# Optimization experiments

Hardware: AMD Instinct MI355X
Metric: run time of the kernel (lower is better)

The kernel has to match this reference:

```python
import jax, jax.numpy as jnp
import numpy as np

N_POINTS = 12288
FEAT_DIM = 16


def setup_inputs() -> dict:
    key = jax.random.key(0)
    feats = jax.random.normal(key, (N_POINTS, FEAT_DIM), dtype=jnp.float32)
    return {"feats": feats, "topK": 1}


def reference(feats, topK):
    """LOGG3D_ATTN eval path for a single point cloud (batch=1).

    feats: [N, D] post-spvcnn point features.
    1) self_attention -> scalar weight per point
    2) weight features, top-k select k = N*topK points
    3) SOP: mean second-order (outer-product) pooling, flatten, L2-normalize.
    """
    N, D = feats.shape
    inv_sqrt_d = 1.0 / jnp.sqrt(jnp.asarray(D, feats.dtype))
    # self-attention over points: [N, N] scores (the ridge-regime hot spot)
    scores = jnp.matmul(feats, feats.T) * inv_sqrt_d          # [N, N]
    attn = jax.nn.softmax(scores, axis=-1)                    # [N, N]
    ctx = jnp.matmul(attn, feats)                             # [N, D]
    weights = jax.nn.sigmoid(jnp.sum(ctx * feats, axis=-1, keepdims=True))  # [N, 1]

    weighted_feat = feats * weights                           # [N, D]
    k = int(N * topK)
    _, top_idx = jax.lax.top_k(weights[:, 0], k)              # [k]
    x = weighted_feat[top_idx][None, :, :]                    # [1, k, D]

    # SOP: mean outer-product pooling (signed_sqrt=False, do_fc=False)
    so = jnp.einsum('bnd,bne->bde', x, x) / k                 # [1, D, D]
    out = so.reshape(1, -1)                                   # [1, D*D]
    out = out / jnp.linalg.norm(out, axis=-1, keepdims=True)
    return out
```

## Files before the change

kernel.cpp:

```cpp
#include <hip/hip_runtime.h>
#include <hip/hip_bf16.h>
#include <math.h>


#define NP 12288
#define JSPLIT 16
#define JCHUNK (NP / JSPLIT)
#define JT 384
#define NTILES (JCHUNK / JT)
#define JGPT (JT / 16)

#define QSCALE 0.3606737602222839f

typedef __attribute__((ext_vector_type(4))) float f32x4;
typedef __attribute__((ext_vector_type(2))) unsigned u32x2;
typedef __attribute__((ext_vector_type(8))) short s16x8;
typedef __attribute__((ext_vector_type(4))) short s16x4;

#if defined(__has_builtin)
#if __has_builtin(__builtin_amdgcn_mfma_f32_16x16x16bf16_1k)
#define HAVE_MFMA16_BUILTIN 1
#endif
#if __has_builtin(__builtin_amdgcn_exp2f)
#define EXP2F(x) __builtin_amdgcn_exp2f(x)
#endif
#endif
#ifndef EXP2F
#define EXP2F(x) exp2f(x)
#endif

static __device__ __forceinline__ f32x4 mfma16(s16x4 a, s16x4 b, f32x4 c) {
#ifdef HAVE_MFMA16_BUILTIN
    return __builtin_amdgcn_mfma_f32_16x16x16bf16_1k(a, b, c, 0, 0, 0);
#else
    f32x4 d;
    asm volatile("s_nop 1\n\t"
                 "v_mfma_f32_16x16x16_bf16 %0, %1, %2, %0"
                 : "=v"(d)
                 : "v"(a), "v"(b), "0"(c));
    return d;
#endif
}

static __device__ __forceinline__ short f2bf(float x) {
    __hip_bfloat16 h = __float2bfloat16(x);
    return __builtin_bit_cast(short, h);
}

static __device__ __forceinline__ s16x4 pack_rhu(f32x4 e) {
    const unsigned u0 = __builtin_bit_cast(unsigned, e[0]) + 0x8000u;
    const unsigned u1 = __builtin_bit_cast(unsigned, e[1]) + 0x8000u;
    const unsigned u2 = __builtin_bit_cast(unsigned, e[2]) + 0x8000u;
    const unsigned u3 = __builtin_bit_cast(unsigned, e[3]) + 0x8000u;
    u32x2 t;
    t[0] = (u0 >> 16) | (u1 & 0xFFFF0000u);
    t[1] = (u2 >> 16) | (u3 & 0xFFFF0000u);
    return __builtin_bit_cast(s16x4, t);
}

__global__ __launch_bounds__(256)
void prep(const float* __restrict__ feats,
          unsigned short* __restrict__ ghi, unsigned short* __restrict__ shi,
          unsigned short* __restrict__ gFt)
{
    __shared__ unsigned short tr[64 * 16];
    const int tid = threadIdx.x;
    const int rowbase = blockIdx.x * 64;

    const f32x4 v = *(const f32x4*)(feats + (size_t)rowbase * 16 + tid * 4);
    s16x4 hv, sv;
    #pragma unroll
    for (int k = 0; k < 4; ++k) {
        hv[k] = f2bf(v[k]);
        sv[k] = f2bf(v[k] * QSCALE);
    }
    *(s16x4*)(ghi + (size_t)rowbase * 16 + tid * 4) = hv;
    *(s16x4*)(shi + (size_t)rowbase * 16 + tid * 4) = sv;
    *(s16x4*)(tr + (tid >> 2) * 16 + (tid & 3) * 4) = hv;
    __syncthreads();

    if (tid < 128) {
        const int p = tid >> 3, q8 = tid & 7;
        s16x8 o;
        #pragma unroll
        for (int e = 0; e < 8; ++e) o[e] = (short)tr[(q8 * 8 + e) * 16 + p];
        *(s16x8*)(gFt + (size_t)p * NP + rowbase + q8 * 8) = o;
    }
}

__global__ __launch_bounds__(256)
void attn_mfma(const unsigned short* __restrict__ ghi,
               const unsigned short* __restrict__ shi,
               const unsigned short* __restrict__ gFt,
               float* __restrict__ ctx_part,
               float* __restrict__ l_part)
{
    __shared__ unsigned short hiT[JT * 16];
    __shared__ unsigned short FtT[16 * JT];

    const int tid = threadIdx.x;
    const int wave = tid >> 6, lane = tid & 63;
    const int il = lane & 15, g = lane >> 4, g4 = g * 4, g8 = g * 8;
    const int js = blockIdx.x & (JSPLIT - 1);
    const int rowblk = blockIdx.x >> 4;
    const int ibase = rowblk * 128 + wave * 32;
    const int jbase = js * JCHUNK;

    const s16x4 bA = *(const s16x4*)(shi + (size_t)(ibase + il) * 16 + g4);
    const s16x4 bB = *(const s16x4*)(shi + (size_t)(ibase + 16 + il) * 16 + g4);

    s16x4 ones; ones[0] = ones[1] = ones[2] = ones[3] = (short)0x3F80;
    const f32x4 kZero = {0.f, 0.f, 0.f, 0.f};
    f32x4 ctxA = kZero, ctxB = kZero, lA = kZero, lB = kZero;

    const char* aBase = (const char*)hiT + ((il * 32 + g8) ^ ((il & 7) << 4));
    const char* vPlane = (const char*)FtT + il * (JT * 2);
    const int vKey = (il & 7) << 4;

    const int fp = tid >> 4, fq = tid & 15;

    for (int ti = 0; ti < NTILES; ++ti) {
        const int jb = jbase + ti * JT;
        {
            const char* gH = (const char*)ghi + (size_t)jb * 32;
            #pragma unroll
            for (int k = 0; k < 3; ++k) {
                const int c = tid + (k << 8);
                s16x8 v = *(const s16x8*)(gH + c * 16);
                *(s16x8*)((char*)hiT + ((c * 16) ^ (((c >> 1) & 7) << 4))) = v;
            }
            const char* gF = (const char*)gFt + (size_t)fp * (NP * 2) + (size_t)jb * 2;
            #pragma unroll
            for (int k = 0; k < 3; ++k) {
                const int cq = fq + (k << 4);
                s16x8 v = *(const s16x8*)(gF + cq * 16);
                *(s16x8*)((char*)FtT + fp * (JT * 2)
                          + ((cq * 16) ^ ((fp & 7) << 4))) = v;
            }
        }
        __syncthreads();

        #pragma unroll 4
        for (int jg = 0; jg < JGPT; ++jg) {
            const s16x4 aS = *(const s16x4*)(aBase + jg * 512);
            const s16x4 aV = *(const s16x4*)(vPlane + (((jg << 5) + g8) ^ vKey));
            const f32x4 sa = mfma16(aS, bA, kZero);
            const f32x4 sb = mfma16(aS, bB, kZero);
            f32x4 ea, eb;
            ea[0] = EXP2F(sa[0]); ea[1] = EXP2F(sa[1]);
            ea[2] = EXP2F(sa[2]); ea[3] = EXP2F(sa[3]);
            eb[0] = EXP2F(sb[0]); eb[1] = EXP2F(sb[1]);
            eb[2] = EXP2F(sb[2]); eb[3] = EXP2F(sb[3]);
            const s16x4 pA = pack_rhu(ea);
            const s16x4 pB = pack_rhu(eb);
            ctxA = mfma16(aV, pA, ctxA);
            lA   = mfma16(ones, pA, lA);
            ctxB = mfma16(aV, pB, ctxB);
            lB   = mfma16(ones, pB, lB);
        }
        __syncthreads();
    }

    asm volatile("s_nop 7\n\ts_nop 7" ::: );

    const int iA = ibase + il, iB = iA + 16;
    *(f32x4*)(ctx_part + ((size_t)js * NP + iA) * 16 + g4) = ctxA;
    *(f32x4*)(ctx_part + ((size_t)js * NP + iB) * 16 + g4) = ctxB;
    if (g == 0) {
        l_part[(size_t)js * NP + iA] = lA[0];
        l_part[(size_t)js * NP + iB] = lB[0];
    }
}

__global__ __launch_bounds__(256)
void weights_sop(const float* __restrict__ feats,
                 const float* __restrict__ ctxp,
                 const float* __restrict__ lp,
                 float* __restrict__ mpart)
{
    __shared__ float gw[64 * 16];
    const int tid = threadIdx.x;
    const int rl = tid >> 2, q = tid & 3, d0 = q * 4;
    const int row = blockIdx.x * 64 + rl;

    f32x4 c = {0.f, 0.f, 0.f, 0.f};
    float l = 0.f;
    #pragma unroll
    for (int js = 0; js < JSPLIT; ++js) {
        c += *(const f32x4*)(ctxp + ((size_t)js * NP + row) * 16 + d0);
        l += lp[(size_t)js * NP + row];
    }
    const f32x4 fv = *(const f32x4*)(feats + (size_t)row * 16 + d0);
    float zp = c[0]*fv[0] + c[1]*fv[1] + c[2]*fv[2] + c[3]*fv[3];
    zp += __shfl_xor(zp, 1, 64);
    zp += __shfl_xor(zp, 2, 64);
    const float z = zp / l;
    const float w = 1.f / (1.f + EXP2F(-z * 1.4426950408889634f));

    f32x4 gv; gv[0] = w*fv[0]; gv[1] = w*fv[1]; gv[2] = w*fv[2]; gv[3] = w*fv[3];
    *(f32x4*)(gw + rl * 16 + d0) = gv;
    __syncthreads();

    const int d = tid >> 4, e = tid & 15;
    float acc = 0.f;
    #pragma unroll 8
    for (int r = 0; r < 64; ++r)
        acc += gw[r * 16 + d] * gw[r * 16 + e];
    mpart[(size_t)blockIdx.x * 256 + tid] = acc;
}

__global__ __launch_bounds__(1024)
void finalize(const float* __restrict__ mpart, float* __restrict__ out)
{
    __shared__ float part[1024];
    __shared__ float red[4];
    const int tid = threadIdx.x;
    const int o = tid & 255, s = tid >> 8;

    float m = 0.f;
    #pragma unroll 4
    for (int b = s; b < 192; b += 4) m += mpart[(size_t)b * 256 + o];
    part[tid] = m;
    __syncthreads();

    if (tid < 256) {
        m = part[tid] + part[tid + 256] + part[tid + 512] + part[tid + 768];
        float ss = m * m;
        #pragma unroll
        for (int msk = 32; msk >= 1; msk >>= 1) ss += __shfl_xor(ss, msk, 64);
        if ((tid & 63) == 0) red[tid >> 6] = ss;
    }
    __syncthreads();
    if (tid < 256) {
        const float tot = red[0] + red[1] + red[2] + red[3];
        out[tid] = m / sqrtf(tot);
    }
}

extern "C" void kernel_launch(void* const* d_in, const int* in_sizes, int n_in,
                              void* d_out, int out_size, void* d_ws, size_t ws_size,
                              hipStream_t stream) {
    (void)n_in; (void)out_size; (void)ws_size;
    const float* feats = (const float*)d_in[0];

    char* w = (char*)d_ws;
    unsigned short* ghi = (unsigned short*)(w);
    unsigned short* shi = (unsigned short*)(w + 393216);
    unsigned short* gFt = (unsigned short*)(w + 786432);
    float* ctxp = (float*)(w + 1179648);
    float* lp   = (float*)(w + 13762560);
    float* mp   = (float*)(w + 14548992);

    prep       <<<192,  256, 0, stream>>>(feats, ghi, shi, gFt);
    attn_mfma  <<<1536, 256, 0, stream>>>(ghi, shi, gFt, ctxp, lp);
    weights_sop<<<192,  256, 0, stream>>>(feats, ctxp, lp, mp);
    finalize   <<<1,    1024, 0, stream>>>(mp, (float*)d_out);
}
```

Measured before the change: 87.77 us.

## Drop LDS staging in attention kernel and load operands directly from global

Removes the shared-memory tiles and the per-tile __syncthreads, so each wave reads its bf16 score and value operands straight from global memory (L1/L2) inside a single loop over the whole j-chunk. This cuts LDS write/read traffic and barrier stalls. The cost is redundant global loads, since the four waves in a block each fetch the same j data, and the loads are 8-byte and strided. The bf16 packing also switches to a v_perm byte permute in place of shift/mask/or.

```diff
diff --git a/kernel.cpp b/kernel.cpp
--- a/kernel.cpp
+++ b/kernel.cpp
@@ -6,9 +6,7 @@
 #define NP 12288
 #define JSPLIT 16
 #define JCHUNK (NP / JSPLIT)
-#define JT 384
-#define NTILES (JCHUNK / JT)
-#define JGPT (JT / 16)
+#define JGTOT (JCHUNK / 16)
 
 #define QSCALE 0.3606737602222839f
 
@@ -23,6 +21,9 @@
 #endif
 #if __has_builtin(__builtin_amdgcn_exp2f)
 #define EXP2F(x) __builtin_amdgcn_exp2f(x)
+#endif
+#if __has_builtin(__builtin_amdgcn_perm)
+#define HAVE_PERM 1
 #endif
 #endif
 #ifndef EXP2F
@@ -53,9 +54,21 @@
     const unsigned u2 = __builtin_bit_cast(unsigned, e[2]) + 0x8000u;
     const unsigned u3 = __builtin_bit_cast(unsigned, e[3]) + 0x8000u;
     u32x2 t;
+#ifdef HAVE_PERM
+    t[0] = __builtin_amdgcn_perm(u1, u0, 0x07060302u);
+    t[1] = __builtin_amdgcn_perm(u3, u2, 0x07060302u);
+#else
     t[0] = (u0 >> 16) | (u1 & 0xFFFF0000u);
     t[1] = (u2 >> 16) | (u3 & 0xFFFF0000u);
+#endif
     return __builtin_bit_cast(s16x4, t);
+}
+
+static __device__ __forceinline__ f32x4 exp4(f32x4 s) {
+    f32x4 e;
+    e[0] = EXP2F(s[0]); e[1] = EXP2F(s[1]);
+    e[2] = EXP2F(s[2]); e[3] = EXP2F(s[3]);
+    return e;
 }
 
 __global__ __launch_bounds__(256)
@@ -95,9 +108,6 @@
                float* __restrict__ ctx_part,
                float* __restrict__ l_part)
 {
-    __shared__ unsigned short hiT[JT * 16];
-    __shared__ unsigned short FtT[16 * JT];
-
     const int tid = threadIdx.x;
     const int wave = tid >> 6, lane = tid & 63;
     const int il = lane & 15, g = lane >> 4, g4 = g * 4, g8 = g * 8;
@@ -113,52 +123,22 @@
     const f32x4 kZero = {0.f, 0.f, 0.f, 0.f};
     f32x4 ctxA = kZero, ctxB = kZero, lA = kZero, lB = kZero;
 
-    const char* aBase = (const char*)hiT + ((il * 32 + g8) ^ ((il & 7) << 4));
-    const char* vPlane = (const char*)FtT + il * (JT * 2);
-    const int vKey = (il & 7) << 4;
-
-    const int fp = tid >> 4, fq = tid & 15;
-
-    for (int ti = 0; ti < NTILES; ++ti) {
-        const int jb = jbase + ti * JT;
-        {
-            const char* gH = (const char*)ghi + (size_t)jb * 32;
-            #pragma unroll
-            for (int k = 0; k < 3; ++k) {
-                const int c = tid + (k << 8);
-                s16x8 v = *(const s16x8*)(gH + c * 16);
-                *(s16x8*)((char*)hiT + ((c * 16) ^ (((c >> 1) & 7) << 4))) = v;
-            }
-            const char* gF = (const char*)gFt + (size_t)fp * (NP * 2) + (size_t)jb * 2;
-            #pragma unroll
-            for (int k = 0; k < 3; ++k) {
-                const int cq = fq + (k << 4);
-                s16x8 v = *(const s16x8*)(gF + cq * 16);
-                *(s16x8*)((char*)FtT + fp * (JT * 2)
-                          + ((cq * 16) ^ ((fp & 7) << 4))) = v;
-            }
-        }
-        __syncthreads();
-
-        #pragma unroll 4
-        for (int jg = 0; jg < JGPT; ++jg) {
-            const s16x4 aS = *(const s16x4*)(aBase + jg * 512);
-            const s16x4 aV = *(const s16x4*)(vPlane + (((jg << 5) + g8) ^ vKey));
-            const f32x4 sa = mfma16(aS, bA, kZero);
-            const f32x4 sb = mfma16(aS, bB, kZero);
-            f32x4 ea, eb;
-            ea[0] = EXP2F(sa[0]); ea[1] = EXP2F(sa[1]);
-            ea[2] = EXP2F(sa[2]); ea[3] = EXP2F(sa[3]);
-            eb[0] = EXP2F(sb[0]); eb[1] = EXP2F(sb[1]);
-            eb[2] = EXP2F(sb[2]); eb[3] = EXP2F(sb[3]);
-            const s16x4 pA = pack_rhu(ea);
-            const s16x4 pB = pack_rhu(eb);
-            ctxA = mfma16(aV, pA, ctxA);
-            lA   = mfma16(ones, pA, lA);
-            ctxB = mfma16(aV, pB, ctxB);
-            lB   = mfma16(ones, pB, lB);
-        }
-        __syncthreads();
+    const char* pS = (const char*)ghi + (size_t)(jbase + il) * 32 + g8;
+    const char* pV = (const char*)gFt + (size_t)il * (NP * 2)
+                     + (size_t)jbase * 2 + g8;
+
+    #pragma unroll 4
+    for (int jg = 0; jg < JGTOT; ++jg) {
+        const s16x4 aS = *(const s16x4*)(pS + (size_t)jg * 512);
+        const s16x4 aV = *(const s16x4*)(pV + (size_t)jg * 32);
+        const f32x4 sa = mfma16(aS, bA, kZero);
+        const f32x4 sb = mfma16(aS, bB, kZero);
+        const s16x4 pA = pack_rhu(exp4(sa));
+        const s16x4 pB = pack_rhu(exp4(sb));
+        ctxA = mfma16(aV, pA, ctxA);
+        lA   = mfma16(ones, pA, lA);
+        ctxB = mfma16(aV, pB, ctxB);
+        lB   = mfma16(ones, pB, lB);
     }
 
     asm volatile("s_nop 7\n\ts_nop 7" ::: );
```

Result: slower. 112.5 us (+28.2%).

## Widen attention blocks to 64 rows per wave and double the key split

Applied to the files above, without the earlier changes.

Each wave now covers 64 query rows (four 16-row MFMA tiles) instead of 32, so each shared-memory key/value fragment load feeds twice as many MFMAs. The key dimension is split 32 ways so each block handles a single 384-key tile, which removes the tile loop and its barriers. The bf16 pack now uses a byte-permute builtin. In exchange the ctx/l partial buffers double in size and the reduction kernel must read twice as many partials, and register pressure rises.

```diff
diff --git a/kernel.cpp b/kernel.cpp
--- a/kernel.cpp
+++ b/kernel.cpp
@@ -4,10 +4,9 @@
 
 
 #define NP 12288
-#define JSPLIT 16
+#define JSPLIT 32
 #define JCHUNK (NP / JSPLIT)
-#define JT 384
-#define NTILES (JCHUNK / JT)
+#define JT JCHUNK
 #define JGPT (JT / 16)
 
 #define QSCALE 0.3606737602222839f
@@ -23,6 +22,9 @@
 #endif
 #if __has_builtin(__builtin_amdgcn_exp2f)
 #define EXP2F(x) __builtin_amdgcn_exp2f(x)
+#endif
+#if __has_builtin(__builtin_amdgcn_perm)
+#define HAVE_PERM 1
 #endif
 #endif
 #ifndef EXP2F
@@ -53,9 +55,21 @@
     const unsigned u2 = __builtin_bit_cast(unsigned, e[2]) + 0x8000u;
     const unsigned u3 = __builtin_bit_cast(unsigned, e[3]) + 0x8000u;
     u32x2 t;
+#ifdef HAVE_PERM
+    t[0] = __builtin_amdgcn_perm(u1, u0, 0x07060302u);
+    t[1] = __builtin_amdgcn_perm(u3, u2, 0x07060302u);
+#else
     t[0] = (u0 >> 16) | (u1 & 0xFFFF0000u);
     t[1] = (u2 >> 16) | (u3 & 0xFFFF0000u);
+#endif
     return __builtin_bit_cast(s16x4, t);
+}
+
+static __device__ __forceinline__ f32x4 exp4(f32x4 s) {
+    f32x4 e;
+    e[0] = EXP2F(s[0]); e[1] = EXP2F(s[1]);
+    e[2] = EXP2F(s[2]); e[3] = EXP2F(s[3]);
+    return e;
 }
 
 __global__ __launch_bounds__(256)
@@ -102,16 +116,20 @@
     const int wave = tid >> 6, lane = tid & 63;
     const int il = lane & 15, g = lane >> 4, g4 = g * 4, g8 = g * 8;
     const int js = blockIdx.x & (JSPLIT - 1);
-    const int rowblk = blockIdx.x >> 4;
-    const int ibase = rowblk * 128 + wave * 32;
+    const int rowblk = blockIdx.x >> 5;
+    const int ibase = rowblk * 256 + wave * 64;
     const int jbase = js * JCHUNK;
 
-    const s16x4 bA = *(const s16x4*)(shi + (size_t)(ibase + il) * 16 + g4);
-    const s16x4 bB = *(const s16x4*)(shi + (size_t)(ibase + 16 + il) * 16 + g4);
+    s16x4 bF[4];
+    #pragma unroll
+    for (int t = 0; t < 4; ++t)
+        bF[t] = *(const s16x4*)(shi + (size_t)(ibase + t * 16 + il) * 16 + g4);
 
     s16x4 ones; ones[0] = ones[1] = ones[2] = ones[3] = (short)0x3F80;
     const f32x4 kZero = {0.f, 0.f, 0.f, 0.f};
-    f32x4 ctxA = kZero, ctxB = kZero, lA = kZero, lB = kZero;
+    f32x4 ctx[4], lacc[4];
+    #pragma unroll
+    for (int t = 0; t < 4; ++t) { ctx[t] = kZero; lacc[t] = kZero; }
 
     const char* aBase = (const char*)hiT + ((il * 32 + g8) ^ ((il & 7) << 4));
     const char* vPlane = (const char*)FtT + il * (JT * 2);
@@ -119,56 +137,45 @@
 
     const int fp = tid >> 4, fq = tid & 15;
 
-    for (int ti = 0; ti < NTILES; ++ti) {
-        const int jb = jbase + ti * JT;
-        {
-            const char* gH = (const char*)ghi + (size_t)jb * 32;
-            #pragma unroll
-            for (int k = 0; k < 3; ++k) {
-                const int c = tid + (k << 8);
-                s16x8 v = *(const s16x8*)(gH + c * 16);
-                *(s16x8*)((char*)hiT + ((c * 16) ^ (((c >> 1) & 7) << 4))) = v;
-            }
-            const char* gF = (const char*)gFt + (size_t)fp * (NP * 2) + (size_t)jb * 2;
-            #pragma unroll
-            for (int k = 0; k < 3; ++k) {
-                const int cq = fq + (k << 4);
-                s16x8 v = *(const s16x8*)(gF + cq * 16);
-                *(s16x8*)((char*)FtT + fp * (JT * 2)
-                          + ((cq * 16) ^ ((fp & 7) << 4))) = v;
-            }
+    {
+        const char* gH = (const char*)ghi + (size_t)jbase * 32;
+        #pragma unroll
+        for (int k = 0; k < 3; ++k) {
+            const int c = tid + (k << 8);
+            s16x8 v = *(const s16x8*)(gH + c * 16);
+            *(s16x8*)((char*)hiT + ((c * 16) ^ (((c >> 1) & 7) << 4))) = v;
         }
-        __syncthreads();
-
-        #pragma unroll 4
-        for (int jg = 0; jg < JGPT; ++jg) {
-            const s16x4 aS = *(const s16x4*)(aBase + jg * 512);
-            const s16x4 aV = *(const s16x4*)(vPlane + (((jg << 5) + g8) ^ vKey));
-            const f32x4 sa = mfma16(aS, bA, kZero);
-            const f32x4 sb = mfma16(aS, bB, kZero);
-            f32x4 ea, eb;
-            ea[0] = EXP2F(sa[0]); ea[1] = EXP2F(sa[1]);
-            ea[2] = EXP2F(sa[2]); ea[3] = EXP2F(sa[3]);
-            eb[0] = EXP2F(sb[0]); eb[1] = EXP2F(sb[1]);
-            eb[2] = EXP2F(sb[2]); eb[3] = EXP2F(sb[3]);
-            const s16x4 pA = pack_rhu(ea);
-            const s16x4 pB = pack_rhu(eb);
-            ctxA = mfma16(aV, pA, ctxA);
-            lA   = mfma16(ones, pA, lA);
-            ctxB = mfma16(aV, pB, ctxB);
-            lB   = mfma16(ones, pB, lB);
+        const char* gF = (const char*)gFt + (size_t)fp * (NP * 2) + (size_t)jbase * 2;
+        #pragma unroll
+        for (int k = 0; k < 3; ++k) {
+            const int cq = fq + (k << 4);
+            s16x8 v = *(const s16x8*)(gF + cq * 16);
+            *(s16x8*)((char*)FtT + fp * (JT * 2)
+                      + ((cq * 16) ^ ((fp & 7) << 4))) = v;
         }
-        __syncthreads();
+    }
+    __syncthreads();
+
+    #pragma unroll 2
+    for (int jg = 0; jg < JGPT; ++jg) {
+        const s16x4 aS = *(const s16x4*)(aBase + jg * 512);
+        const s16x4 aV = *(const s16x4*)(vPlane + (((jg << 5) + g8) ^ vKey));
+        #pragma unroll
+        for (int t = 0; t < 4; ++t) {
+            const f32x4 s = mfma16(aS, bF[t], kZero);
+            const s16x4 p = pack_rhu(exp4(s));
+            ctx[t]  = mfma16(aV, p, ctx[t]);
+            lacc[t] = mfma16(ones, p, lacc[t]);
+        }
     }
 
     asm volatile("s_nop 7\n\ts_nop 7" ::: );
 
-    const int iA = ibase + il, iB = iA + 16;
-    *(f32x4*)(ctx_part + ((size_t)js * NP + iA) * 16 + g4) = ctxA;
-    *(f32x4*)(ctx_part + ((size_t)js * NP + iB) * 16 + g4) = ctxB;
-    if (g == 0) {
-        l_part[(size_t)js * NP + iA] = lA[0];
-        l_part[(size_t)js * NP + iB] = lB[0];
+    #pragma unroll
+    for (int t = 0; t < 4; ++t) {
+        const int iT = ibase + t * 16 + il;
+        *(f32x4*)(ctx_part + ((size_t)js * NP + iT) * 16 + g4) = ctx[t];
+        if (g == 0) l_part[(size_t)js * NP + iT] = lacc[t][0];
     }
 }
 
@@ -185,7 +192,7 @@
 
     f32x4 c = {0.f, 0.f, 0.f, 0.f};
     float l = 0.f;
-    #pragma unroll
+    #pragma unroll 8
     for (int js = 0; js < JSPLIT; ++js) {
         c += *(const f32x4*)(ctxp + ((size_t)js * NP + row) * 16 + d0);
         l += lp[(size_t)js * NP + row];
@@ -248,8 +255,8 @@
     unsigned short* shi = (unsigned short*)(w + 393216);
     unsigned short* gFt = (unsigned short*)(w + 786432);
     float* ctxp = (float*)(w + 1179648);
-    float* lp   = (float*)(w + 13762560);
-    float* mp   = (float*)(w + 14548992);
+    float* lp   = (float*)(w + 26345472);
+    float* mp   = (float*)(w + 27918336);
 
     prep       <<<192,  256, 0, stream>>>(feats, ghi, shi, gFt);
     attn_mfma  <<<1536, 256, 0, stream>>>(ghi, shi, gFt, ctxp, lp);
```

New measurement: 94.57 us. 7.7% more time.
